# Performance work log

Measured on AMD Instinct MI355X. Metric: run time of the kernel, lower is better.

The kernel has to match this reference:

```python
import jax, jax.numpy as jnp
import numpy as np

N = 50000      # nodes
E = 800000     # edges (avg degree 16)
D_IN, D_H, D_OUT = 128, 256, 128


def setup_inputs() -> dict:
    key = jax.random.key(0)
    ks = jax.random.split(key, 8)
    x = jax.random.normal(ks[0], (N, D_IN), dtype=jnp.float32)
    edge_index = jax.random.randint(ks[1], (2, E), 0, N, dtype=jnp.int64)
    s1 = 1.0 / np.sqrt(D_IN).astype(np.float32)
    s2 = 1.0 / np.sqrt(D_H).astype(np.float32)
    return {
        "x": x,
        "edge_index": edge_index,
        "W1l": jax.random.normal(ks[2], (D_H, D_IN), jnp.float32) * s1,
        "b1l": jnp.zeros((D_H,), jnp.float32),
        "W1r": jax.random.normal(ks[3], (D_H, D_IN), jnp.float32) * s1,
        "W2l": jax.random.normal(ks[4], (D_OUT, D_H), jnp.float32) * s2,
        "b2l": jnp.zeros((D_OUT,), jnp.float32),
        "W2r": jax.random.normal(ks[5], (D_OUT, D_H), jnp.float32) * s2,
    }


def sage_conv(x, src, dst, Wl, bl, Wr):
    # mean-aggregate source features into destination nodes
    agg = jax.ops.segment_sum(x[src], dst, num_segments=N)           # [N, d_in]
    deg = jax.ops.segment_sum(jnp.ones((src.shape[0],), x.dtype), dst, num_segments=N)
    mean = agg / jnp.maximum(deg, 1.0)[:, None]
    # lin_l(mean_agg) + lin_r(x_root); lin_r has no bias (PyG SAGEConv default)
    return mean @ Wl.T + bl + x @ Wr.T


def reference(x, edge_index, W1l, b1l, W1r, W2l, b2l, W2r):
    src, dst = edge_index[0], edge_index[1]
    h = sage_conv(x, src, dst, W1l, b1l, W1r)
    h = jax.nn.relu(h)  # dropout inactive in eval mode
    return sage_conv(h, src, dst, W2l, b2l, W2r)
```

## Files before the change

### kernel.cpp

```cpp
#include <hip/hip_runtime.h>


typedef __attribute__((ext_vector_type(8))) short bf16x8;
typedef __attribute__((ext_vector_type(4))) float floatx4;

__device__ inline unsigned short f2b(float f) {
  unsigned int x = __float_as_uint(f);
  unsigned int r = (x + 0x7fffu + ((x >> 16) & 1u)) >> 16;
  return (unsigned short)r;
}
__device__ inline float blo(unsigned int u) { return __uint_as_float(u << 16); }
__device__ inline float bhi(unsigned int u) { return __uint_as_float(u & 0xffff0000u); }

__global__ void prep_kernel(const float* __restrict__ x,
                            const float* __restrict__ W1l, const float* __restrict__ W1r,
                            const float* __restrict__ W2l, const float* __restrict__ W2r,
                            unsigned short* __restrict__ Wc1, unsigned short* __restrict__ Wc2,
                            unsigned short* __restrict__ A1,
                            int* __restrict__ cnt, int* __restrict__ off, int N, int E) {
  int i = blockIdx.x * blockDim.x + threadIdx.x;
  if (i < 65536) {
    int j = i >> 8, k = i & 255;
    float v1 = (k < 128) ? W1l[j * 128 + k] : W1r[j * 128 + (k - 128)];
    Wc1[i] = f2b(v1);
    float v2 = (j < 128) ? W2l[j * 256 + k] : W2r[(j - 128) * 256 + k];
    Wc2[i] = f2b(v2);
  }
  if (i < N) cnt[i] = 0;
  if (i == 0) off[N] = E;
  if (i < N * 32) {
    int n = i >> 5, c = (i & 31) * 4;
    float4 v = *(const float4*)(x + (size_t)n * 128 + c);
    uint2 p;
    p.x = (unsigned int)f2b(v.x) | ((unsigned int)f2b(v.y) << 16);
    p.y = (unsigned int)f2b(v.z) | ((unsigned int)f2b(v.w) << 16);
    *(uint2*)(A1 + (size_t)n * 256 + 128 + c) = p;
  }
}

__global__ void hist_kernel(const int* __restrict__ dst, int* __restrict__ cnt,
                            int* __restrict__ rank, int E) {
  int i = blockIdx.x * blockDim.x + threadIdx.x;
  int e = i * 4;
  if (e + 3 < E) {
    int4 d = *(const int4*)(dst + e);
    int4 r;
    r.x = atomicAdd(&cnt[d.x], 1);
    r.y = atomicAdd(&cnt[d.y], 1);
    r.z = atomicAdd(&cnt[d.z], 1);
    r.w = atomicAdd(&cnt[d.w], 1);
    *(int4*)(rank + e) = r;
  } else {
    for (; e < E; e++) rank[e] = atomicAdd(&cnt[dst[e]], 1);
  }
}

__global__ __launch_bounds__(1024) void scan_blocks_kernel(const int* __restrict__ cnt,
                                                           int* __restrict__ off,
                                                           int* __restrict__ bsum, int N) {
  __shared__ int wsum[16];
  __shared__ int wincl[16];
  const int tid = threadIdx.x;
  const int lane = tid & 63;
  const int wv = tid >> 6;
  const int i = blockIdx.x * 1024 + tid;
  const int v = (i < N) ? cnt[i] : 0;
  int s = v;
#pragma unroll
  for (int o = 1; o < 64; o <<= 1) {
    int t = __shfl_up(s, o, 64);
    if (lane >= o) s += t;
  }
  if (lane == 63) wsum[wv] = s;
  __syncthreads();
  if (tid < 16) {
    int ws = wsum[tid];
#pragma unroll
    for (int o = 1; o < 16; o <<= 1) {
      int t = __shfl_up(ws, o, 16);
      if ((tid & 15) >= o) ws += t;
    }
    wincl[tid] = ws;
  }
  __syncthreads();
  const int wo = wv ? wincl[wv - 1] : 0;
  if (i < N) off[i] = wo + s - v;
  if (tid == 1023) bsum[blockIdx.x] = wo + s;
}

__global__ __launch_bounds__(1024) void scan_add_kernel(int* __restrict__ off,
                                                        const int* __restrict__ bsum, int N, int SB) {
  __shared__ int bofs[64];
  const int tid = threadIdx.x;
  if (tid < 64) {
    int v = (tid < SB) ? bsum[tid] : 0;
    int s = v;
#pragma unroll
    for (int o = 1; o < 64; o <<= 1) {
      int t = __shfl_up(s, o, 64);
      if (tid >= o) s += t;
    }
    bofs[tid] = s - v;
  }
  __syncthreads();
  int i = blockIdx.x * 1024 + tid;
  if (i < N) off[i] = off[i] + bofs[blockIdx.x];
}

__global__ void fill_kernel(const int* __restrict__ src, const int* __restrict__ dst,
                            const int* __restrict__ rank, const int* __restrict__ off,
                            int* __restrict__ csr, int E) {
  int i = blockIdx.x * blockDim.x + threadIdx.x;
  int e = i * 4;
  if (e + 3 < E) {
    int4 d = *(const int4*)(dst + e);
    int4 r = *(const int4*)(rank + e);
    int4 s = *(const int4*)(src + e);
    csr[off[d.x] + r.x] = s.x;
    csr[off[d.y] + r.y] = s.y;
    csr[off[d.z] + r.z] = s.z;
    csr[off[d.w] + r.w] = s.w;
  } else {
    for (; e < E; e++) csr[off[dst[e]] + rank[e]] = src[e];
  }
}

__global__ void gather1_kernel(const unsigned short* __restrict__ feat,
                               const int* __restrict__ csr, const int* __restrict__ off,
                               unsigned short* __restrict__ ob, int N) {
  int wid = (blockIdx.x * blockDim.x + threadIdx.x) >> 6;
  if (wid >= N) return;
  const int lane = threadIdx.x & 63;
  const int s0 = off[wid], s1 = off[wid + 1];
  float a0 = 0.f, a1 = 0.f;
  for (int base = s0; base < s1; base += 64) {
    const int cnt = min(64, s1 - base);
    int my = (lane < cnt) ? csr[base + lane] : 0;
    int k = 0;
    for (; k + 8 <= cnt; k += 8) {
      int i0 = __shfl(my, k);
      int i1 = __shfl(my, k + 1);
      int i2 = __shfl(my, k + 2);
      int i3 = __shfl(my, k + 3);
      int i4 = __shfl(my, k + 4);
      int i5 = __shfl(my, k + 5);
      int i6 = __shfl(my, k + 6);
      int i7 = __shfl(my, k + 7);
      unsigned u0 = ((const unsigned*)(feat + (size_t)i0 * 256))[lane];
      unsigned u1 = ((const unsigned*)(feat + (size_t)i1 * 256))[lane];
      unsigned u2 = ((const unsigned*)(feat + (size_t)i2 * 256))[lane];
      unsigned u3 = ((const unsigned*)(feat + (size_t)i3 * 256))[lane];
      unsigned u4 = ((const unsigned*)(feat + (size_t)i4 * 256))[lane];
      unsigned u5 = ((const unsigned*)(feat + (size_t)i5 * 256))[lane];
      unsigned u6 = ((const unsigned*)(feat + (size_t)i6 * 256))[lane];
      unsigned u7 = ((const unsigned*)(feat + (size_t)i7 * 256))[lane];
      a0 += blo(u0); a1 += bhi(u0);
      a0 += blo(u1); a1 += bhi(u1);
      a0 += blo(u2); a1 += bhi(u2);
      a0 += blo(u3); a1 += bhi(u3);
      a0 += blo(u4); a1 += bhi(u4);
      a0 += blo(u5); a1 += bhi(u5);
      a0 += blo(u6); a1 += bhi(u6);
      a0 += blo(u7); a1 += bhi(u7);
    }
    for (; k + 2 <= cnt; k += 2) {
      int i0 = __shfl(my, k);
      int i1 = __shfl(my, k + 1);
      unsigned u0 = ((const unsigned*)(feat + (size_t)i0 * 256))[lane];
      unsigned u1 = ((const unsigned*)(feat + (size_t)i1 * 256))[lane];
      a0 += blo(u0); a1 += bhi(u0);
      a0 += blo(u1); a1 += bhi(u1);
    }
    if (k < cnt) {
      int i0 = __shfl(my, k);
      unsigned u0 = ((const unsigned*)(feat + (size_t)i0 * 256))[lane];
      a0 += blo(u0); a1 += bhi(u0);
    }
  }
  const float inv = 1.0f / fmaxf((float)(s1 - s0), 1.0f);
  unsigned p = (unsigned)f2b(a0 * inv) | ((unsigned)f2b(a1 * inv) << 16);
  ((unsigned*)(ob + (size_t)wid * 256))[lane] = p;
}

__global__ void gather2_kernel(const unsigned short* __restrict__ t,
                               const int* __restrict__ csr, const int* __restrict__ off,
                               float* __restrict__ out, int N) {
  int wid = (blockIdx.x * blockDim.x + threadIdx.x) >> 6;
  if (wid >= N) return;
  const int lane = threadIdx.x & 63;
  const int s0 = off[wid], s1 = off[wid + 1];
  float2* op = (float2*)(out + (size_t)wid * 128) + lane;
  float2 r = *op;
  float a0 = 0.f, a1 = 0.f;
  for (int base = s0; base < s1; base += 64) {
    const int cnt = min(64, s1 - base);
    int my = (lane < cnt) ? csr[base + lane] : 0;
    int k = 0;
    for (; k + 8 <= cnt; k += 8) {
      int i0 = __shfl(my, k);
      int i1 = __shfl(my, k + 1);
      int i2 = __shfl(my, k + 2);
      int i3 = __shfl(my, k + 3);
      int i4 = __shfl(my, k + 4);
      int i5 = __shfl(my, k + 5);
      int i6 = __shfl(my, k + 6);
      int i7 = __shfl(my, k + 7);
      unsigned u0 = ((const unsigned*)(t + (size_t)i0 * 128))[lane];
      unsigned u1 = ((const unsigned*)(t + (size_t)i1 * 128))[lane];
      unsigned u2 = ((const unsigned*)(t + (size_t)i2 * 128))[lane];
      unsigned u3 = ((const unsigned*)(t + (size_t)i3 * 128))[lane];
      unsigned u4 = ((const unsigned*)(t + (size_t)i4 * 128))[lane];
      unsigned u5 = ((const unsigned*)(t + (size_t)i5 * 128))[lane];
      unsigned u6 = ((const unsigned*)(t + (size_t)i6 * 128))[lane];
      unsigned u7 = ((const unsigned*)(t + (size_t)i7 * 128))[lane];
      a0 += blo(u0); a1 += bhi(u0);
      a0 += blo(u1); a1 += bhi(u1);
      a0 += blo(u2); a1 += bhi(u2);
      a0 += blo(u3); a1 += bhi(u3);
      a0 += blo(u4); a1 += bhi(u4);
      a0 += blo(u5); a1 += bhi(u5);
      a0 += blo(u6); a1 += bhi(u6);
      a0 += blo(u7); a1 += bhi(u7);
    }
    for (; k + 2 <= cnt; k += 2) {
      int i0 = __shfl(my, k);
      int i1 = __shfl(my, k + 1);
      unsigned u0 = ((const unsigned*)(t + (size_t)i0 * 128))[lane];
      unsigned u1 = ((const unsigned*)(t + (size_t)i1 * 128))[lane];
      a0 += blo(u0); a1 += bhi(u0);
      a0 += blo(u1); a1 += bhi(u1);
    }
    if (k < cnt) {
      int i0 = __shfl(my, k);
      unsigned u0 = ((const unsigned*)(t + (size_t)i0 * 128))[lane];
      a0 += blo(u0); a1 += bhi(u0);
    }
  }
  const float inv = 1.0f / fmaxf((float)(s1 - s0), 1.0f);
  r.x += a0 * inv;
  r.y += a1 * inv;
  *op = r;
}

__global__ __launch_bounds__(512, 2)
void gemm_fused(const unsigned short* __restrict__ A, const unsigned short* __restrict__ Wc1,
                const unsigned short* __restrict__ Wc2,
                const float* __restrict__ b1, const float* __restrict__ b2,
                unsigned short* __restrict__ tb, float* __restrict__ out, int M) {
  constexpr int LDA = 264;
  __shared__ __align__(16) unsigned short AH[128 * LDA];
  const int t = threadIdx.x;
  const int lane = t & 63;
  const int wave = t >> 6;
  const int wn = wave * 32;
  const int l15 = lane & 15;
  const int quad = lane >> 4;
  const int m_blk = blockIdx.x * 128;

  bf16x8 wr[2][8];
#pragma unroll
  for (int nt = 0; nt < 2; nt++) {
    const unsigned short* wp = Wc1 + (size_t)(wn + nt * 16 + l15) * 256 + quad * 8;
#pragma unroll
    for (int c = 0; c < 8; c++) wr[nt][c] = *(const bf16x8*)(wp + c * 32);
  }
  const float bv0 = b1[wn + l15];
  const float bv1 = b1[wn + 16 + l15];

#pragma unroll
  for (int i = 0; i < 8; i++) {
    int idx = t + 512 * i;
    int row = idx >> 5, cc = (idx & 31) * 8;
    int ar = m_blk + row;
    if (ar >= M) ar = M - 1;
    *(uint4*)(AH + row * LDA + cc) = *(const uint4*)(A + (size_t)ar * 256 + cc);
  }
  __syncthreads();

  floatx4 acc[8][2] = {};
#pragma unroll
  for (int c = 0; c < 8; c++) {
    bf16x8 af[8];
#pragma unroll
    for (int mt = 0; mt < 8; mt++)
      af[mt] = *(const bf16x8*)(AH + (mt * 16 + l15) * LDA + c * 32 + quad * 8);
#pragma unroll
    for (int mt = 0; mt < 8; mt++) {
      acc[mt][0] = __builtin_amdgcn_mfma_f32_16x16x32_bf16(af[mt], wr[0][c], acc[mt][0], 0, 0, 0);
      acc[mt][1] = __builtin_amdgcn_mfma_f32_16x16x32_bf16(af[mt], wr[1][c], acc[mt][1], 0, 0, 0);
    }
  }

#pragma unroll
  for (int nt = 0; nt < 2; nt++) {
    const unsigned short* wp = Wc2 + (size_t)(wn + nt * 16 + l15) * 256 + quad * 8;
#pragma unroll
    for (int c = 0; c < 8; c++) wr[nt][c] = *(const bf16x8*)(wp + c * 32);
  }
  const float cv0 = (wn >= 128) ? b2[wn - 128 + l15] : 0.f;
  const float cv1 = (wn >= 128) ? b2[wn - 112 + l15] : 0.f;
  __syncthreads();

#pragma unroll
  for (int mt = 0; mt < 8; mt++) {
#pragma unroll
    for (int nt = 0; nt < 2; nt++) {
      const int jl = wn + nt * 16 + l15;
      const float bv = nt ? bv1 : bv0;
#pragma unroll
      for (int r = 0; r < 4; r++) {
        const int row = mt * 16 + quad * 4 + r;
        AH[row * LDA + jl] = f2b(fmaxf(acc[mt][nt][r] + bv, 0.f));
      }
    }
  }
  __syncthreads();

#pragma unroll
  for (int mt = 0; mt < 8; mt++) {
    acc[mt][0] = (floatx4){0.f, 0.f, 0.f, 0.f};
    acc[mt][1] = (floatx4){0.f, 0.f, 0.f, 0.f};
  }
#pragma unroll
  for (int c = 0; c < 8; c++) {
    bf16x8 af[8];
#pragma unroll
    for (int mt = 0; mt < 8; mt++)
      af[mt] = *(const bf16x8*)(AH + (mt * 16 + l15) * LDA + c * 32 + quad * 8);
#pragma unroll
    for (int mt = 0; mt < 8; mt++) {
      acc[mt][0] = __builtin_amdgcn_mfma_f32_16x16x32_bf16(af[mt], wr[0][c], acc[mt][0], 0, 0, 0);
      acc[mt][1] = __builtin_amdgcn_mfma_f32_16x16x32_bf16(af[mt], wr[1][c], acc[mt][1], 0, 0, 0);
    }
  }

#pragma unroll
  for (int mt = 0; mt < 8; mt++) {
#pragma unroll
    for (int nt = 0; nt < 2; nt++) {
      const int j = wn + nt * 16 + l15;
      const float bv = nt ? cv1 : cv0;
#pragma unroll
      for (int r = 0; r < 4; r++) {
        const int node = m_blk + mt * 16 + quad * 4 + r;
        if (node >= M) continue;
        const float v = acc[mt][nt][r];
        if (j < 128) {
          tb[(size_t)node * 128 + j] = f2b(v);
        } else {
          out[(size_t)node * 128 + (j - 128)] = v + bv;
        }
      }
    }
  }
}

extern "C" void kernel_launch(void* const* d_in, const int* in_sizes, int n_in,
                              void* d_out, int out_size, void* d_ws, size_t ws_size,
                              hipStream_t stream) {
  const float* x   = (const float*)d_in[0];
  const int*  eidx = (const int*)d_in[1];
  const float* W1l = (const float*)d_in[2];
  const float* b1l = (const float*)d_in[3];
  const float* W1r = (const float*)d_in[4];
  const float* W2l = (const float*)d_in[5];
  const float* b2l = (const float*)d_in[6];
  const float* W2r = (const float*)d_in[7];
  float* out = (float*)d_out;

  const int N = in_sizes[0] / 128;
  const int E = in_sizes[1] / 2;
  const int* src = eidx;
  const int* dst = eidx + E;

  int* cnt  = (int*)d_ws;
  int* off  = cnt + N;
  int* bsum = off + N + 1;
  int* rank = bsum + 64;
  int* csr  = rank + E;
  size_t ioff = ((size_t)(N + N + 1 + 64 + 2 * E) * 4 + 15) & ~(size_t)15;
  unsigned short* A1  = (unsigned short*)((char*)d_ws + ioff);
  unsigned short* tb  = A1 + (size_t)N * 256;
  unsigned short* Wc1 = tb + (size_t)N * 128;
  unsigned short* Wc2 = Wc1 + 65536;

  const int SB = (N + 1023) / 1024;

  prep_kernel<<<(N * 32 + 255) / 256, 256, 0, stream>>>(x, W1l, W1r, W2l, W2r,
                                                        Wc1, Wc2, A1, cnt, off, N, E);
  hist_kernel<<<(E / 4 + 255) / 256, 256, 0, stream>>>(dst, cnt, rank, E);
  scan_blocks_kernel<<<SB, 1024, 0, stream>>>(cnt, off, bsum, N);
  scan_add_kernel<<<SB, 1024, 0, stream>>>(off, bsum, N, SB);
  fill_kernel<<<(E / 4 + 255) / 256, 256, 0, stream>>>(src, dst, rank, off, csr, E);

  const int gblocks = (N + 3) / 4;
  gather1_kernel<<<gblocks, 256, 0, stream>>>(A1 + 128, csr, off, A1, N);

  gemm_fused<<<(N + 127) / 128, 512, 0, stream>>>(A1, Wc1, Wc2, b1l, b2l, tb, out, N);

  gather2_kernel<<<gblocks, 256, 0, stream>>>(tb, csr, off, out, N);
}
```

Measured before the change: 262.7 us.

## Store CSR indices as 16-bit and gather two neighbors per wave with 8-byte loads

The edge rank and CSR source arrays become unsigned short instead of int, which halves the index traffic in the histogram, fill and gather kernels. Each gather wave now splits into two half-waves that handle different neighbors, each lane loading a uint2 of features, 16 neighbors per unrolled step. The two halves are combined with a cross-half shuffle reduction at the end. This relies on node ids and per-node degree fitting in 16 bits, which holds for N=50000 but would silently corrupt results for larger graphs.

Result: no change. 260.5 us (-0.8%).

```diff
diff --git a/kernel.cpp b/kernel.cpp
--- a/kernel.cpp
+++ b/kernel.cpp
@@ -39,19 +39,19 @@
 }
 
 __global__ void hist_kernel(const int* __restrict__ dst, int* __restrict__ cnt,
-                            int* __restrict__ rank, int E) {
+                            unsigned short* __restrict__ rank, int E) {
   int i = blockIdx.x * blockDim.x + threadIdx.x;
   int e = i * 4;
   if (e + 3 < E) {
     int4 d = *(const int4*)(dst + e);
-    int4 r;
-    r.x = atomicAdd(&cnt[d.x], 1);
-    r.y = atomicAdd(&cnt[d.y], 1);
-    r.z = atomicAdd(&cnt[d.z], 1);
-    r.w = atomicAdd(&cnt[d.w], 1);
-    *(int4*)(rank + e) = r;
+    ushort4 r;
+    r.x = (unsigned short)atomicAdd(&cnt[d.x], 1);
+    r.y = (unsigned short)atomicAdd(&cnt[d.y], 1);
+    r.z = (unsigned short)atomicAdd(&cnt[d.z], 1);
+    r.w = (unsigned short)atomicAdd(&cnt[d.w], 1);
+    *(ushort4*)(rank + e) = r;
   } else {
-    for (; e < E; e++) rank[e] = atomicAdd(&cnt[dst[e]], 1);
+    for (; e < E; e++) rank[e] = (unsigned short)atomicAdd(&cnt[dst[e]], 1);
   }
 }
 
@@ -108,138 +108,137 @@
 }
 
 __global__ void fill_kernel(const int* __restrict__ src, const int* __restrict__ dst,
-                            const int* __restrict__ rank, const int* __restrict__ off,
-                            int* __restrict__ csr, int E) {
+                            const unsigned short* __restrict__ rank, const int* __restrict__ off,
+                            unsigned short* __restrict__ csr, int E) {
   int i = blockIdx.x * blockDim.x + threadIdx.x;
   int e = i * 4;
   if (e + 3 < E) {
     int4 d = *(const int4*)(dst + e);
-    int4 r = *(const int4*)(rank + e);
+    ushort4 r = *(const ushort4*)(rank + e);
     int4 s = *(const int4*)(src + e);
-    csr[off[d.x] + r.x] = s.x;
-    csr[off[d.y] + r.y] = s.y;
-    csr[off[d.z] + r.z] = s.z;
-    csr[off[d.w] + r.w] = s.w;
+    csr[off[d.x] + r.x] = (unsigned short)s.x;
+    csr[off[d.y] + r.y] = (unsigned short)s.y;
+    csr[off[d.z] + r.z] = (unsigned short)s.z;
+    csr[off[d.w] + r.w] = (unsigned short)s.w;
   } else {
-    for (; e < E; e++) csr[off[dst[e]] + rank[e]] = src[e];
+    for (; e < E; e++) csr[off[dst[e]] + rank[e]] = (unsigned short)src[e];
   }
 }
 
 __global__ void gather1_kernel(const unsigned short* __restrict__ feat,
-                               const int* __restrict__ csr, const int* __restrict__ off,
+                               const unsigned short* __restrict__ csr, const int* __restrict__ off,
                                unsigned short* __restrict__ ob, int N) {
   int wid = (blockIdx.x * blockDim.x + threadIdx.x) >> 6;
   if (wid >= N) return;
   const int lane = threadIdx.x & 63;
+  const int half = lane >> 5;
+  const int c = lane & 31;
   const int s0 = off[wid], s1 = off[wid + 1];
-  float a0 = 0.f, a1 = 0.f;
+  float a0 = 0.f, a1 = 0.f, a2 = 0.f, a3 = 0.f;
   for (int base = s0; base < s1; base += 64) {
     const int cnt = min(64, s1 - base);
-    int my = (lane < cnt) ? csr[base + lane] : 0;
+    int my = (lane < cnt) ? (int)csr[base + lane] : 0;
     int k = 0;
-    for (; k + 8 <= cnt; k += 8) {
-      int i0 = __shfl(my, k);
-      int i1 = __shfl(my, k + 1);
-      int i2 = __shfl(my, k + 2);
-      int i3 = __shfl(my, k + 3);
-      int i4 = __shfl(my, k + 4);
-      int i5 = __shfl(my, k + 5);
-      int i6 = __shfl(my, k + 6);
-      int i7 = __shfl(my, k + 7);
-      unsigned u0 = ((const unsigned*)(feat + (size_t)i0 * 256))[lane];
-      unsigned u1 = ((const unsigned*)(feat + (size_t)i1 * 256))[lane];
-      unsigned u2 = ((const unsigned*)(feat + (size_t)i2 * 256))[lane];
-      unsigned u3 = ((const unsigned*)(feat + (size_t)i3 * 256))[lane];
-      unsigned u4 = ((const unsigned*)(feat + (size_t)i4 * 256))[lane];
-      unsigned u5 = ((const unsigned*)(feat + (size_t)i5 * 256))[lane];
-      unsigned u6 = ((const unsigned*)(feat + (size_t)i6 * 256))[lane];
-      unsigned u7 = ((const unsigned*)(feat + (size_t)i7 * 256))[lane];
-      a0 += blo(u0); a1 += bhi(u0);
-      a0 += blo(u1); a1 += bhi(u1);
-      a0 += blo(u2); a1 += bhi(u2);
-      a0 += blo(u3); a1 += bhi(u3);
-      a0 += blo(u4); a1 += bhi(u4);
-      a0 += blo(u5); a1 += bhi(u5);
-      a0 += blo(u6); a1 += bhi(u6);
-      a0 += blo(u7); a1 += bhi(u7);
+    for (; k + 16 <= cnt; k += 16) {
+      int r[8];
+#pragma unroll
+      for (int p = 0; p < 8; p++) r[p] = __shfl(my, k + 2 * p + half);
+      uint2 u[8];
+#pragma unroll
+      for (int p = 0; p < 8; p++)
+        u[p] = ((const uint2*)(feat + (size_t)r[p] * 256))[c];
+#pragma unroll
+      for (int p = 0; p < 8; p++) {
+        a0 += blo(u[p].x); a1 += bhi(u[p].x);
+        a2 += blo(u[p].y); a3 += bhi(u[p].y);
+      }
     }
     for (; k + 2 <= cnt; k += 2) {
-      int i0 = __shfl(my, k);
-      int i1 = __shfl(my, k + 1);
-      unsigned u0 = ((const unsigned*)(feat + (size_t)i0 * 256))[lane];
-      unsigned u1 = ((const unsigned*)(feat + (size_t)i1 * 256))[lane];
-      a0 += blo(u0); a1 += bhi(u0);
-      a0 += blo(u1); a1 += bhi(u1);
+      int r0 = __shfl(my, k + half);
+      uint2 u = ((const uint2*)(feat + (size_t)r0 * 256))[c];
+      a0 += blo(u.x); a1 += bhi(u.x);
+      a2 += blo(u.y); a3 += bhi(u.y);
     }
     if (k < cnt) {
-      int i0 = __shfl(my, k);
-      unsigned u0 = ((const unsigned*)(feat + (size_t)i0 * 256))[lane];
-      a0 += blo(u0); a1 += bhi(u0);
-    }
-  }
-  const float inv = 1.0f / fmaxf((float)(s1 - s0), 1.0f);
-  unsigned p = (unsigned)f2b(a0 * inv) | ((unsigned)f2b(a1 * inv) << 16);
-  ((unsigned*)(ob + (size_t)wid * 256))[lane] = p;
+      int r0 = __shfl(my, k);
+      if (half == 0) {
+        uint2 u = ((const uint2*)(feat + (size_t)r0 * 256))[c];
+        a0 += blo(u.x); a1 += bhi(u.x);
+        a2 += blo(u.y); a3 += bhi(u.y);
+      }
+    }
+  }
+  a0 += __shfl_xor(a0, 32);
+  a1 += __shfl_xor(a1, 32);
+  a2 += __shfl_xor(a2, 32);
+  a3 += __shfl_xor(a3, 32);
+  if (half == 0) {
+    const float inv = 1.0f / fmaxf((float)(s1 - s0), 1.0f);
+    uint2 p;
+    p.x = (unsigned)f2b(a0 * inv) | ((unsigned)f2b(a1 * inv) << 16);
+    p.y = (unsigned)f2b(a2 * inv) | ((unsigned)f2b(a3 * inv) << 16);
+    ((uint2*)(ob + (size_t)wid * 256))[c] = p;
+  }
 }
 
 __global__ void gather2_kernel(const unsigned short* __restrict__ t,
-                               const int* __restrict__ csr, const int* __restrict__ off,
+                               const unsigned short* __restrict__ csr, const int* __restrict__ off,
                                float* __restrict__ out, int N) {
   int wid = (blockIdx.x * blockDim.x + threadIdx.x) >> 6;
   if (wid >= N) return;
   const int lane = threadIdx.x & 63;
+  const int half = lane >> 5;
+  const int c = lane & 31;
   const int s0 = off[wid], s1 = off[wid + 1];
-  float2* op = (float2*)(out + (size_t)wid * 128) + lane;
-  float2 r = *op;
-  float a0 = 0.f, a1 = 0.f;
+  float4* op = (float4*)(out + (size_t)wid * 128) + c;
+  float4 rr;
+  if (half == 0) rr = *op;
+  float a0 = 0.f, a1 = 0.f, a2 = 0.f, a3 = 0.f;
   for (int base = s0; base < s1; base += 64) {
     const int cnt = min(64, s1 - base);
-    int my = (lane < cnt) ? csr[base + lane] : 0;
+    int my = (lane < cnt) ? (int)csr[base + lane] : 0;
     int k = 0;
-    for (; k + 8 <= cnt; k += 8) {
-      int i0 = __shfl(my, k);
-      int i1 = __shfl(my, k + 1);
-      int i2 = __shfl(my, k + 2);
-      int i3 = __shfl(my, k + 3);
-      int i4 = __shfl(my, k + 4);
-      int i5 = __shfl(my, k + 5);
-      int i6 = __shfl(my, k + 6);
-      int i7 = __shfl(my, k + 7);
-      unsigned u0 = ((const unsigned*)(t + (size_t)i0 * 128))[lane];
-      unsigned u1 = ((const unsigned*)(t + (size_t)i1 * 128))[lane];
-      unsigned u2 = ((const unsigned*)(t + (size_t)i2 * 128))[lane];
-      unsigned u3 = ((const unsigned*)(t + (size_t)i3 * 128))[lane];
-      unsigned u4 = ((const unsigned*)(t + (size_t)i4 * 128))[lane];
-      unsigned u5 = ((const unsigned*)(t + (size_t)i5 * 128))[lane];
-      unsigned u6 = ((const unsigned*)(t + (size_t)i6 * 128))[lane];
-      unsigned u7 = ((const unsigned*)(t + (size_t)i7 * 128))[lane];
-      a0 += blo(u0); a1 += bhi(u0);
-      a0 += blo(u1); a1 += bhi(u1);
-      a0 += blo(u2); a1 += bhi(u2);
-      a0 += blo(u3); a1 += bhi(u3);
-      a0 += blo(u4); a1 += bhi(u4);
-      a0 += blo(u5); a1 += bhi(u5);
-      a0 += blo(u6); a1 += bhi(u6);
-      a0 += blo(u7); a1 += bhi(u7);
+    for (; k + 16 <= cnt; k += 16) {
+      int r[8];
+#pragma unroll
+      for (int p = 0; p < 8; p++) r[p] = __shfl(my, k + 2 * p + half);
+      uint2 u[8];
+#pragma unroll
+      for (int p = 0; p < 8; p++)
+        u[p] = ((const uint2*)(t + (size_t)r[p] * 128))[c];
+#pragma unroll
+      for (int p = 0; p < 8; p++) {
+        a0 += blo(u[p].x); a1 += bhi(u[p].x);
+        a2 += blo(u[p].y); a3 += bhi(u[p].y);
+      }
     }
     for (; k + 2 <= cnt; k += 2) {
-      int i0 = __shfl(my, k);
-      int i1 = __shfl(my, k + 1);
-      unsigned u0 = ((const unsigned*)(t + (size_t)i0 * 128))[lane];
-      unsigned u1 = ((const unsigned*)(t + (size_t)i1 * 128))[lane];
-      a0 += blo(u0); a1 += bhi(u0);
-      a0 += blo(u1); a1 += bhi(u1);
+      int r0 = __shfl(my, k + half);
+      uint2 u = ((const uint2*)(t + (size_t)r0 * 128))[c];
+      a0 += blo(u.x); a1 += bhi(u.x);
+      a2 += blo(u.y); a3 += bhi(u.y);
     }
     if (k < cnt) {
-      int i0 = __shfl(my, k);
-      unsigned u0 = ((const unsigned*)(t + (size_t)i0 * 128))[lane];
-      a0 += blo(u0); a1 += bhi(u0);
-    }
-  }
-  const float inv = 1.0f / fmaxf((float)(s1 - s0), 1.0f);
-  r.x += a0 * inv;
-  r.y += a1 * inv;
-  *op = r;
+      int r0 = __shfl(my, k);
+      if (half == 0) {
+        uint2 u = ((const uint2*)(t + (size_t)r0 * 128))[c];
+        a0 += blo(u.x); a1 += bhi(u.x);
+        a2 += blo(u.y); a3 += bhi(u.y);
+      }
+    }
+  }
+  a0 += __shfl_xor(a0, 32);
+  a1 += __shfl_xor(a1, 32);
+  a2 += __shfl_xor(a2, 32);
+  a3 += __shfl_xor(a3, 32);
+  if (half == 0) {
+    const float inv = 1.0f / fmaxf((float)(s1 - s0), 1.0f);
+    rr.x += a0 * inv;
+    rr.y += a1 * inv;
+    rr.z += a2 * inv;
+    rr.w += a3 * inv;
+    *op = rr;
+  }
 }
 
 __global__ __launch_bounds__(512, 2)
@@ -376,9 +375,10 @@
   int* cnt  = (int*)d_ws;
   int* off  = cnt + N;
   int* bsum = off + N + 1;
-  int* rank = bsum + 64;
-  int* csr  = rank + E;
-  size_t ioff = ((size_t)(N + N + 1 + 64 + 2 * E) * 4 + 15) & ~(size_t)15;
+  size_t cbase = (((size_t)(N + N + 1 + 64) * 4) + 15) & ~(size_t)15;
+  unsigned short* rank = (unsigned short*)((char*)d_ws + cbase);
+  unsigned short* csr  = rank + E;
+  size_t ioff = (cbase + (size_t)E * 4 + 15) & ~(size_t)15;
   unsigned short* A1  = (unsigned short*)((char*)d_ws + ioff);
   unsigned short* tb  = A1 + (size_t)N * 256;
   unsigned short* Wc1 = tb + (size_t)N * 128;
```
